# Kernel optimization log

Hardware: AMD Instinct MI355X
Metric: run time of the kernel (lower is better)

## Reference

```python
import jax, jax.numpy as jnp
import numpy as np

SIGMAS = [15, 80, 250]  # hardcoded defaults in retinex_MSR


def _gauss_k1d(sigma):
    # matches get_gauss_kernel(sigma, dim=1)
    ksize = int(np.floor(sigma * 6) / 2) * 2 + 1
    k = np.arange(ksize, dtype=np.float32) - ksize // 2
    k = np.exp(-k ** 2 / (2.0 * sigma ** 2))
    k /= k.sum()
    return jnp.asarray(k)


def _gauss_blur(x, k1d):
    # x: (N, 1, H, W); separable blur with zero padding, same as F.conv2d
    K = k1d.shape[0]
    pad = K // 2
    dn = ('NCHW', 'OIHW', 'NCHW')
    kv = k1d.reshape(1, 1, K, 1)
    kh = k1d.reshape(1, 1, 1, K)
    x = jax.lax.conv_general_dilated(x, kv, (1, 1), [(pad, pad), (0, 0)], dimension_numbers=dn)
    x = jax.lax.conv_general_dilated(x, kh, (1, 1), [(0, 0), (pad, pad)], dimension_numbers=dn)
    return x


def setup_inputs() -> dict:
    key = jax.random.key(0)
    img = jax.random.uniform(key, (16, 3, 512, 512), dtype=jnp.float32)
    return {"img": img}


def reference(img):
    B, C, H, W = img.shape
    # all channels processed identically as single-channel depthwise convs:
    # fold channels into batch for one big conv per sigma
    x = img.astype(jnp.float32).reshape(B * C, 1, H, W)
    w = 1.0 / len(SIGMAS)  # default equal weights summing to 1
    r = jnp.zeros((B * C, 1, H, W), dtype=jnp.float32)
    for sigma in SIGMAS:
        r = r + jnp.log(_gauss_blur(x, _gauss_k1d(sigma)) + 1.0) * w
    r = r.reshape(B, C, H, W)
    # per-channel min-max stretch, global over batch and spatial dims
    mmin = r.min(axis=(0, 2, 3), keepdims=True)
    mmax = r.max(axis=(0, 2, 3), keepdims=True)
    return (r - mmin) / (mmax - mmin)
```

## Files before the change

### kernel.cpp

```cpp
#include <hip/hip_runtime.h>
#include <math.h>


#define NSL 48

#define W0_OFF 0
#define W1_OFF 512
#define W2_OFF 1280
#define MM_OFF 2816
#define G16_BYTE_OFF 16384
#define X16_BYTE_OFF 1589248
#define T16_BYTE_OFF 26755072

typedef _Float16 half8 __attribute__((ext_vector_type(8)));
typedef float f32x4 __attribute__((ext_vector_type(4)));

__device__ __forceinline__ void gload16(const void* g, void* l) {
  __builtin_amdgcn_global_load_lds(
      (const __attribute__((address_space(1))) void*)g,
      (__attribute__((address_space(3))) void*)l, 16, 0, 0);
}

#define WAITV4() asm volatile("s_waitcnt vmcnt(4)" ::: "memory")
#define WAITV0() asm volatile("s_waitcnt vmcnt(0)" ::: "memory")
#define SCHEDB() __builtin_amdgcn_sched_barrier(0)
#define BARRIER() __builtin_amdgcn_s_barrier()

__global__ void wkern(float* __restrict__ ws) {
  __shared__ float red[256];
  const int s = blockIdx.x;
  const int Ks[3] = {91, 481, 1501};
  const float sg[3] = {15.f, 80.f, 250.f};
  const int off[3] = {W0_OFF, W1_OFF, W2_OFF};
  const int alloc[3] = {512, 768, 1536};
  const int K = Ks[s], A = alloc[s];
  float* wb = ws + off[s];
  const int t = threadIdx.x;
  for (int i = t; i < A; i += 256) wb[i] = 0.f;
  __syncthreads();
  const float inv2s2 = 1.f / (2.f * sg[s] * sg[s]);
  float part = 0.f;
  for (int i = t; i < K; i += 256) {
    const float d = (float)(i - K / 2);
    const float e = __expf(-d * d * inv2s2);
    wb[16 + i] = e;
    part += e;
  }
  red[t] = part;
  __syncthreads();
  for (int st = 128; st > 0; st >>= 1) {
    if (t < st) red[t] += red[t + st];
    __syncthreads();
  }
  const float inv = 1.f / red[0];
  for (int i = t; i < K; i += 256) wb[16 + i] *= inv;
}

__global__ void mm_init(unsigned* __restrict__ mm) {
  const int t = threadIdx.x;
  if (t < 3) mm[t] = 0xFFFFFFFFu;
  else if (t < 6) mm[t] = 0u;
}

__global__ void gkern(const float* __restrict__ ws, _Float16* __restrict__ gb) {
  const int y = blockIdx.x;
  const int s = blockIdx.y;
  const int Rs[3] = {45, 240, 750};
  const int off[3] = {W0_OFF, W1_OFF, W2_OFF};
  const float* w = ws + off[s] + 16;
  _Float16* g = gb + ((size_t)s << 18) + ((size_t)y << 9);
  const int R = Rs[s], K = 2 * R + 1;
  for (int x = threadIdx.x; x < 512; x += 256) {
    const int i = x - y + R;
    const float v = (i >= 0 && i < K) ? w[i] : 0.f;
    g[x] = (_Float16)v;
  }
}

__global__ __launch_bounds__(256) void xconv(const float* __restrict__ X,
                                             _Float16* __restrict__ X16) {
  const size_t i = ((size_t)blockIdx.x * 256 + threadIdx.x) << 3;
  const float4 v0 = *reinterpret_cast<const float4*>(X + i);
  const float4 v1 = *reinterpret_cast<const float4*>(X + i + 4);
  half8 h;
  h[0] = (_Float16)v0.x; h[1] = (_Float16)v0.y;
  h[2] = (_Float16)v0.z; h[3] = (_Float16)v0.w;
  h[4] = (_Float16)v1.x; h[5] = (_Float16)v1.y;
  h[6] = (_Float16)v1.z; h[7] = (_Float16)v1.w;
  *reinterpret_cast<half8*>(X16 + i) = h;
}

#define STAGE_P(buf)                                 \
  do {                                               \
    gload16(pA0, &As[buf][t << 3]);                  \
    gload16(pA1, &As[buf][(256 + t) << 3]);          \
    gload16(pB0, &Bs[buf][t << 3]);                  \
    gload16(pB1, &Bs[buf][(256 + t) << 3]);          \
    pA0 += 32; pA1 += 32; pB0 += 32; pB1 += 32;      \
  } while (0)

#define FRAGS_AND_MFMA(buf)                                                         \
  do {                                                                              \
    half8 af[4], bf[4];                                                             \
    _Pragma("unroll") for (int f = 0; f < 4; ++f) {                                 \
      af[f] = *reinterpret_cast<const half8*>(                                      \
          &As[buf][(((wr << 6) + (f << 4) + lr) << 5) + (lg << 3)]);                \
      bf[f] = *reinterpret_cast<const half8*>(                                      \
          &Bs[buf][(((wc << 6) + (f << 4) + lr) << 5) + (lg << 3)]);                \
    }                                                                               \
    _Pragma("unroll") for (int fm = 0; fm < 4; ++fm)                                \
        _Pragma("unroll") for (int fn = 0; fn < 4; ++fn)                            \
        acc[fm][fn] = __builtin_amdgcn_mfma_f32_16x16x32_f16(af[fm], bf[fn],        \
                                                             acc[fm][fn], 0, 0, 0); \
  } while (0)

#define K_PIPELINE_LOOP()                                                           \
  do {                                                                              \
    const int row_ = t >> 2;                                                        \
    const int c8_ = (t & 3) << 3;                                                   \
    const _Float16* pA0 =                                                           \
        Ap + ((size_t)(bm + row_) << 9) + (klo << 5) + c8_;                         \
    const _Float16* pA1 = pA0 + ((size_t)64 << 9);                                  \
    const _Float16* pB0 =                                                           \
        Bp + ((size_t)(bn + row_) << 9) + (klo << 5) + c8_;                         \
    const _Float16* pB1 = pB0 + ((size_t)64 << 9);                                  \
    STAGE_P(0);                                                                     \
    STAGE_P(1);                                                                     \
    int cb = 0;                                                                     \
    for (int kt = klo; kt <= khi; ++kt) {                                           \
      if (kt < khi) { WAITV4(); } else { WAITV0(); }                                \
      SCHEDB();                                                                     \
      BARRIER();                                                                    \
      SCHEDB();                                                                     \
      if (kt + 2 <= khi) {                                                          \
        const int sb = (cb + 2 >= 3) ? cb - 1 : cb + 2;                             \
        STAGE_P(sb);                                                                \
      }                                                                             \
      FRAGS_AND_MFMA(cb);                                                           \
      cb = (cb == 2) ? 0 : cb + 1;                                                  \
    }                                                                               \
  } while (0)

__global__ __launch_bounds__(256) void gemm1_k(const _Float16* __restrict__ X16,
                                               const _Float16* __restrict__ G16,
                                               _Float16* __restrict__ T16) {
  __shared__ __align__(16) _Float16 As[3][128 * 32];
  __shared__ __align__(16) _Float16 Bs[3][128 * 32];
  const int t = threadIdx.x;
  const int lane = t & 63, wave = t >> 6;
  const int wr = wave >> 1, wc = wave & 1;
  const int lr = lane & 15, lg = lane >> 4;
  const int idx = blockIdx.x;
  const int idy = blockIdx.y;
  const int idx12 = idy % 12;
  const int q = idx + ((idy / 12) << 3);
  const int bn = (q & 3) << 7;
  const int slice = q >> 2;
  const int bm = (idx12 & 3) << 7;
  const int s = idx12 >> 2;
  const int Rs[3] = {45, 240, 750};
  const int R = Rs[s];
  const _Float16* Ap = G16 + ((size_t)s << 18);
  const _Float16* Bp = X16 + ((size_t)slice << 18);
  _Float16* Tout = T16 + ((size_t)(s * NSL + slice) << 18);

  int klo = bm - R;
  klo = (klo > 0 ? klo : 0) >> 5;
  int khi = bm + 127 + R;
  if (khi > 511) khi = 511;
  khi >>= 5;

  f32x4 acc[4][4];
#pragma unroll
  for (int i = 0; i < 4; ++i)
#pragma unroll
    for (int j = 0; j < 4; ++j) acc[i][j] = (f32x4){0.f, 0.f, 0.f, 0.f};

  K_PIPELINE_LOOP();

#pragma unroll
  for (int fm = 0; fm < 4; ++fm)
#pragma unroll
    for (int fn = 0; fn < 4; ++fn) {
      const int a0 = bm + (wr << 6) + (fm << 4) + (lg << 2);
      const int b0 = bn + (wc << 6) + (fn << 4) + lr;
#pragma unroll
      for (int j = 0; j < 4; ++j)
        Tout[((size_t)(a0 + j) << 9) + b0] = (_Float16)acc[fm][fn][j];
    }
}

__global__ __launch_bounds__(256) void gemm2_k(const _Float16* __restrict__ G16,
                                               const _Float16* __restrict__ T16,
                                               float* __restrict__ out,
                                               unsigned* __restrict__ mm) {
  __shared__ __align__(16) _Float16 As[3][128 * 32];
  __shared__ __align__(16) _Float16 Bs[3][128 * 32];
  __shared__ float smn[4], smx[4];
  const int t = threadIdx.x;
  const int lane = t & 63, wave = t >> 6;
  const int wr = wave >> 1, wc = wave & 1;
  const int lr = lane & 15, lg = lane >> 4;
  const int idx = blockIdx.x;
  const int idy = blockIdx.y;
  const int bm = (idy & 3) << 7;
  const int q = idx + ((idy >> 2) << 3);
  const int bn = (q & 3) << 7;
  const int slice = q >> 2;
  const float w3 = 1.f / 3.f;
  const int Rs[3] = {45, 240, 750};

  f32x4 res[4][4];
#pragma unroll
  for (int i = 0; i < 4; ++i)
#pragma unroll
    for (int j = 0; j < 4; ++j) res[i][j] = (f32x4){0.f, 0.f, 0.f, 0.f};

#pragma unroll 1
  for (int s = 0; s < 3; ++s) {
    const int R = Rs[s];
    const _Float16* Ap = G16 + ((size_t)s << 18);
    const _Float16* Bp = T16 + ((size_t)(s * NSL + slice) << 18);
    int klo = bm - R;
    klo = (klo > 0 ? klo : 0) >> 5;
    int khi = bm + 127 + R;
    if (khi > 511) khi = 511;
    khi >>= 5;

    f32x4 acc[4][4];
#pragma unroll
    for (int i = 0; i < 4; ++i)
#pragma unroll
      for (int j = 0; j < 4; ++j) acc[i][j] = (f32x4){0.f, 0.f, 0.f, 0.f};

    BARRIER();
    K_PIPELINE_LOOP();

#pragma unroll
    for (int fm = 0; fm < 4; ++fm)
#pragma unroll
      for (int fn = 0; fn < 4; ++fn)
#pragma unroll
        for (int j = 0; j < 4; ++j)
          res[fm][fn][j] += w3 * __logf(acc[fm][fn][j] + 1.f);
  }

  float mn = 3.4e38f, mx = -3.4e38f;
#pragma unroll
  for (int fm = 0; fm < 4; ++fm)
#pragma unroll
    for (int fn = 0; fn < 4; ++fn) {
      const int rb = bm + (wr << 6) + (fm << 4) + (lg << 2);
      const int cg = bn + (wc << 6) + (fn << 4) + lr;
      float* op = out + ((size_t)slice << 18) + ((size_t)rb << 9) + cg;
#pragma unroll
      for (int j = 0; j < 4; ++j) {
        const float v = res[fm][fn][j];
        op[j << 9] = v;
        mn = fminf(mn, v);
        mx = fmaxf(mx, v);
      }
    }
#pragma unroll
  for (int off = 32; off > 0; off >>= 1) {
    mn = fminf(mn, __shfl_xor(mn, off));
    mx = fmaxf(mx, __shfl_xor(mx, off));
  }
  if (lane == 0) {
    smn[wave] = mn;
    smx[wave] = mx;
  }
  __syncthreads();
  if (t == 0) {
    mn = fminf(fminf(smn[0], smn[1]), fminf(smn[2], smn[3]));
    mx = fmaxf(fmaxf(smx[0], smx[1]), fmaxf(smx[2], smx[3]));
    const int ch = slice % 3;
    atomicMin(&mm[ch], __float_as_uint(mn));
    atomicMax(&mm[3 + ch], __float_as_uint(mx));
  }
}

__global__ __launch_bounds__(256) void norm_k(float* __restrict__ r,
                                              const unsigned* __restrict__ mm) {
  const int b = blockIdx.x;
  const int slice = b >> 4;
  const int piece = b & 15;
  const int ch = slice % 3;
  const float mn = __uint_as_float(mm[ch]);
  const float mx = __uint_as_float(mm[3 + ch]);
  const float inv = 1.f / (mx - mn);
  float* p = r + ((size_t)slice << 18) + (piece << 14);
  const int t = threadIdx.x;
  for (int q = 0; q < 16; ++q) {
    float4 v = *reinterpret_cast<const float4*>(&p[(q * 256 + t) << 2]);
    v.x = (v.x - mn) * inv;
    v.y = (v.y - mn) * inv;
    v.z = (v.z - mn) * inv;
    v.w = (v.w - mn) * inv;
    *reinterpret_cast<float4*>(&p[(q * 256 + t) << 2]) = v;
  }
}

extern "C" void kernel_launch(void* const* d_in, const int* in_sizes, int n_in,
                              void* d_out, int out_size, void* d_ws, size_t ws_size,
                              hipStream_t stream) {
  const float* img = (const float*)d_in[0];
  float* out = (float*)d_out;
  float* wsf = (float*)d_ws;
  unsigned* mm = (unsigned*)(wsf + MM_OFF);
  _Float16* G16 = (_Float16*)((char*)d_ws + G16_BYTE_OFF);
  _Float16* X16 = (_Float16*)((char*)d_ws + X16_BYTE_OFF);
  _Float16* T16 = (_Float16*)((char*)d_ws + T16_BYTE_OFF);

  wkern<<<3, 256, 0, stream>>>(wsf);
  mm_init<<<1, 64, 0, stream>>>(mm);
  gkern<<<dim3(512, 3), 256, 0, stream>>>(wsf, G16);
  xconv<<<6144, 256, 0, stream>>>(img, X16);

  gemm1_k<<<dim3(8, 288), 256, 0, stream>>>(X16, G16, T16);
  gemm2_k<<<dim3(8, 96), 256, 0, stream>>>(G16, T16, out, mm);

  norm_k<<<768, 256, 0, stream>>>(out, mm);
}
```

Before: 156.6 us.

## Switch GEMM K-loop to 64-wide tiles with double buffering and syncthreads

The banded GEMM K-loop now stages 64-wide K tiles instead of 32-wide ones, using two LDS buffers in place of three. The manual vmcnt waits and sched barriers are replaced by a plain __syncthreads each iteration. This halves the number of loop iterations and barriers per tile, which cuts per-iteration overhead. In exchange it loses the deeper prefetch, shares one barrier between the wait and the next load, and makes the band edges coarser, so some extra zero-weight K work is done.

```diff
diff --git a/kernel.cpp b/kernel.cpp
--- a/kernel.cpp
+++ b/kernel.cpp
@@ -20,11 +20,6 @@
       (const __attribute__((address_space(1))) void*)g,
       (__attribute__((address_space(3))) void*)l, 16, 0, 0);
 }
-
-#define WAITV4() asm volatile("s_waitcnt vmcnt(4)" ::: "memory")
-#define WAITV0() asm volatile("s_waitcnt vmcnt(0)" ::: "memory")
-#define SCHEDB() __builtin_amdgcn_sched_barrier(0)
-#define BARRIER() __builtin_amdgcn_s_barrier()
 
 __global__ void wkern(float* __restrict__ ws) {
   __shared__ float red[256];
@@ -90,62 +85,64 @@
   *reinterpret_cast<half8*>(X16 + i) = h;
 }
 
-#define STAGE_P(buf)                                 \
-  do {                                               \
-    gload16(pA0, &As[buf][t << 3]);                  \
-    gload16(pA1, &As[buf][(256 + t) << 3]);          \
-    gload16(pB0, &Bs[buf][t << 3]);                  \
-    gload16(pB1, &Bs[buf][(256 + t) << 3]);          \
-    pA0 += 32; pA1 += 32; pB0 += 32; pB1 += 32;      \
+#define STAGE8(buf)                                    \
+  do {                                                 \
+    gload16(pA0, &As[buf][t << 3]);                    \
+    gload16(pA1, &As[buf][(256 + t) << 3]);            \
+    gload16(pA2, &As[buf][(512 + t) << 3]);            \
+    gload16(pA3, &As[buf][(768 + t) << 3]);            \
+    gload16(pB0, &Bs[buf][t << 3]);                    \
+    gload16(pB1, &Bs[buf][(256 + t) << 3]);            \
+    gload16(pB2, &Bs[buf][(512 + t) << 3]);            \
+    gload16(pB3, &Bs[buf][(768 + t) << 3]);            \
+    pA0 += 64; pA1 += 64; pA2 += 64; pA3 += 64;        \
+    pB0 += 64; pB1 += 64; pB2 += 64; pB3 += 64;        \
   } while (0)
 
 #define FRAGS_AND_MFMA(buf)                                                         \
   do {                                                                              \
-    half8 af[4], bf[4];                                                             \
-    _Pragma("unroll") for (int f = 0; f < 4; ++f) {                                 \
-      af[f] = *reinterpret_cast<const half8*>(                                      \
-          &As[buf][(((wr << 6) + (f << 4) + lr) << 5) + (lg << 3)]);                \
-      bf[f] = *reinterpret_cast<const half8*>(                                      \
-          &Bs[buf][(((wc << 6) + (f << 4) + lr) << 5) + (lg << 3)]);                \
+    _Pragma("unroll") for (int ks = 0; ks < 2; ++ks) {                              \
+      half8 af[4], bf[4];                                                           \
+      _Pragma("unroll") for (int f = 0; f < 4; ++f) {                               \
+        af[f] = *reinterpret_cast<const half8*>(                                    \
+            &As[buf][(((wr << 6) + (f << 4) + lr) << 6) + (ks << 5) + (lg << 3)]);  \
+        bf[f] = *reinterpret_cast<const half8*>(                                    \
+            &Bs[buf][(((wc << 6) + (f << 4) + lr) << 6) + (ks << 5) + (lg << 3)]);  \
+      }                                                                             \
+      _Pragma("unroll") for (int fm = 0; fm < 4; ++fm)                              \
+          _Pragma("unroll") for (int fn = 0; fn < 4; ++fn)                          \
+          acc[fm][fn] = __builtin_amdgcn_mfma_f32_16x16x32_f16(af[fm], bf[fn],      \
+                                                               acc[fm][fn], 0, 0, 0); \
     }                                                                               \
-    _Pragma("unroll") for (int fm = 0; fm < 4; ++fm)                                \
-        _Pragma("unroll") for (int fn = 0; fn < 4; ++fn)                            \
-        acc[fm][fn] = __builtin_amdgcn_mfma_f32_16x16x32_f16(af[fm], bf[fn],        \
-                                                             acc[fm][fn], 0, 0, 0); \
   } while (0)
 
 #define K_PIPELINE_LOOP()                                                           \
   do {                                                                              \
-    const int row_ = t >> 2;                                                        \
-    const int c8_ = (t & 3) << 3;                                                   \
-    const _Float16* pA0 =                                                           \
-        Ap + ((size_t)(bm + row_) << 9) + (klo << 5) + c8_;                         \
-    const _Float16* pA1 = pA0 + ((size_t)64 << 9);                                  \
-    const _Float16* pB0 =                                                           \
-        Bp + ((size_t)(bn + row_) << 9) + (klo << 5) + c8_;                         \
-    const _Float16* pB1 = pB0 + ((size_t)64 << 9);                                  \
-    STAGE_P(0);                                                                     \
-    STAGE_P(1);                                                                     \
+    const int rA_ = t >> 3;                                                         \
+    const int g8_ = (t & 7) << 3;                                                   \
+    const _Float16* pA0 = Ap + ((size_t)(bm + rA_) << 9) + (klo << 6) + g8_;        \
+    const _Float16* pA1 = pA0 + ((size_t)32 << 9);                                  \
+    const _Float16* pA2 = pA0 + ((size_t)64 << 9);                                  \
+    const _Float16* pA3 = pA0 + ((size_t)96 << 9);                                  \
+    const _Float16* pB0 = Bp + ((size_t)(bn + rA_) << 9) + (klo << 6) + g8_;        \
+    const _Float16* pB1 = pB0 + ((size_t)32 << 9);                                  \
+    const _Float16* pB2 = pB0 + ((size_t)64 << 9);                                  \
+    const _Float16* pB3 = pB0 + ((size_t)96 << 9);                                  \
+    STAGE8(0);                                                                      \
     int cb = 0;                                                                     \
     for (int kt = klo; kt <= khi; ++kt) {                                           \
-      if (kt < khi) { WAITV4(); } else { WAITV0(); }                                \
-      SCHEDB();                                                                     \
-      BARRIER();                                                                    \
-      SCHEDB();                                                                     \
-      if (kt + 2 <= khi) {                                                          \
-        const int sb = (cb + 2 >= 3) ? cb - 1 : cb + 2;                             \
-        STAGE_P(sb);                                                                \
-      }                                                                             \
+      __syncthreads();                                                              \
+      if (kt < khi) STAGE8(cb ^ 1);                                                 \
       FRAGS_AND_MFMA(cb);                                                           \
-      cb = (cb == 2) ? 0 : cb + 1;                                                  \
+      cb ^= 1;                                                                      \
     }                                                                               \
   } while (0)
 
 __global__ __launch_bounds__(256) void gemm1_k(const _Float16* __restrict__ X16,
                                                const _Float16* __restrict__ G16,
                                                _Float16* __restrict__ T16) {
-  __shared__ __align__(16) _Float16 As[3][128 * 32];
-  __shared__ __align__(16) _Float16 Bs[3][128 * 32];
+  __shared__ __align__(16) _Float16 As[2][128 * 64];
+  __shared__ __align__(16) _Float16 Bs[2][128 * 64];
   const int t = threadIdx.x;
   const int lane = t & 63, wave = t >> 6;
   const int wr = wave >> 1, wc = wave & 1;
@@ -165,10 +162,10 @@
   _Float16* Tout = T16 + ((size_t)(s * NSL + slice) << 18);
 
   int klo = bm - R;
-  klo = (klo > 0 ? klo : 0) >> 5;
+  klo = (klo > 0 ? klo : 0) >> 6;
   int khi = bm + 127 + R;
   if (khi > 511) khi = 511;
-  khi >>= 5;
+  khi >>= 6;
 
   f32x4 acc[4][4];
 #pragma unroll
@@ -194,8 +191,8 @@
                                                const _Float16* __restrict__ T16,
                                                float* __restrict__ out,
                                                unsigned* __restrict__ mm) {
-  __shared__ __align__(16) _Float16 As[3][128 * 32];
-  __shared__ __align__(16) _Float16 Bs[3][128 * 32];
+  __shared__ __align__(16) _Float16 As[2][128 * 64];
+  __shared__ __align__(16) _Float16 Bs[2][128 * 64];
   __shared__ float smn[4], smx[4];
   const int t = threadIdx.x;
   const int lane = t & 63, wave = t >> 6;
@@ -222,10 +219,10 @@
     const _Float16* Ap = G16 + ((size_t)s << 18);
     const _Float16* Bp = T16 + ((size_t)(s * NSL + slice) << 18);
     int klo = bm - R;
-    klo = (klo > 0 ? klo : 0) >> 5;
+    klo = (klo > 0 ? klo : 0) >> 6;
     int khi = bm + 127 + R;
     if (khi > 511) khi = 511;
-    khi >>= 5;
+    khi >>= 6;
 
     f32x4 acc[4][4];
 #pragma unroll
@@ -233,7 +230,7 @@
 #pragma unroll
       for (int j = 0; j < 4; ++j) acc[i][j] = (f32x4){0.f, 0.f, 0.f, 0.f};
 
-    BARRIER();
+    __syncthreads();
     K_PIPELINE_LOOP();
 
 #pragma unroll
```

Result: slower. 165.4 us (+5.6%).

## Use 64-wide K tiles with XOR-swizzled LDS and double buffering in gemm2

Applied to the files above, without the earlier changes.

The second banded GEMM now stages K tiles of 64 instead of 32, double-buffered instead of triple-buffered. Global-to-LDS loads use an XOR-swizzled column chunk so fragment reads avoid LDS bank conflicts. Explicit vmcnt waits are replaced by plain __syncthreads. This halves the barrier count per K range and cuts bank conflicts, but the band bounds are coarser (more zero-band work), LDS use rises to 64KB, and only one tile of prefetch is in flight.

```diff
diff --git a/kernel.cpp b/kernel.cpp
--- a/kernel.cpp
+++ b/kernel.cpp
@@ -90,7 +90,7 @@
   *reinterpret_cast<half8*>(X16 + i) = h;
 }
 
-#define STAGE_P(buf)                                 \
+#define STAGE_P1(buf)                                \
   do {                                               \
     gload16(pA0, &As[buf][t << 3]);                  \
     gload16(pA1, &As[buf][(256 + t) << 3]);          \
@@ -99,7 +99,7 @@
     pA0 += 32; pA1 += 32; pB0 += 32; pB1 += 32;      \
   } while (0)
 
-#define FRAGS_AND_MFMA(buf)                                                         \
+#define FRAGS_MFMA1(buf)                                                            \
   do {                                                                              \
     half8 af[4], bf[4];                                                             \
     _Pragma("unroll") for (int f = 0; f < 4; ++f) {                                 \
@@ -114,7 +114,7 @@
                                                              acc[fm][fn], 0, 0, 0); \
   } while (0)
 
-#define K_PIPELINE_LOOP()                                                           \
+#define K_LOOP1()                                                                   \
   do {                                                                              \
     const int row_ = t >> 2;                                                        \
     const int c8_ = (t & 3) << 3;                                                   \
@@ -124,8 +124,8 @@
     const _Float16* pB0 =                                                           \
         Bp + ((size_t)(bn + row_) << 9) + (klo << 5) + c8_;                         \
     const _Float16* pB1 = pB0 + ((size_t)64 << 9);                                  \
-    STAGE_P(0);                                                                     \
-    STAGE_P(1);                                                                     \
+    STAGE_P1(0);                                                                    \
+    STAGE_P1(1);                                                                    \
     int cb = 0;                                                                     \
     for (int kt = klo; kt <= khi; ++kt) {                                           \
       if (kt < khi) { WAITV4(); } else { WAITV0(); }                                \
@@ -134,9 +134,9 @@
       SCHEDB();                                                                     \
       if (kt + 2 <= khi) {                                                          \
         const int sb = (cb + 2 >= 3) ? cb - 1 : cb + 2;                             \
-        STAGE_P(sb);                                                                \
+        STAGE_P1(sb);                                                               \
       }                                                                             \
-      FRAGS_AND_MFMA(cb);                                                           \
+      FRAGS_MFMA1(cb);                                                              \
       cb = (cb == 2) ? 0 : cb + 1;                                                  \
     }                                                                               \
   } while (0)
@@ -176,7 +176,7 @@
 #pragma unroll
     for (int j = 0; j < 4; ++j) acc[i][j] = (f32x4){0.f, 0.f, 0.f, 0.f};
 
-  K_PIPELINE_LOOP();
+  K_LOOP1();
 
 #pragma unroll
   for (int fm = 0; fm < 4; ++fm)
@@ -189,13 +189,68 @@
         Tout[((size_t)(a0 + j) << 9) + b0] = (_Float16)acc[fm][fn][j];
     }
 }
+
+#define STAGE8SW(buf)                                  \
+  do {                                                 \
+    gload16(pA0, &As[buf][t << 3]);                    \
+    gload16(pA1, &As[buf][(256 + t) << 3]);            \
+    gload16(pA2, &As[buf][(512 + t) << 3]);            \
+    gload16(pA3, &As[buf][(768 + t) << 3]);            \
+    gload16(pB0, &Bs[buf][t << 3]);                    \
+    gload16(pB1, &Bs[buf][(256 + t) << 3]);            \
+    gload16(pB2, &Bs[buf][(512 + t) << 3]);            \
+    gload16(pB3, &Bs[buf][(768 + t) << 3]);            \
+    pA0 += 64; pA1 += 64; pA2 += 64; pA3 += 64;        \
+    pB0 += 64; pB1 += 64; pB2 += 64; pB3 += 64;        \
+  } while (0)
+
+#define FRAGS_MFMA2(buf)                                                            \
+  do {                                                                              \
+    _Pragma("unroll") for (int ks = 0; ks < 2; ++ks) {                              \
+      half8 af[4], bf[4];                                                           \
+      _Pragma("unroll") for (int f = 0; f < 4; ++f) {                               \
+        af[f] = *reinterpret_cast<const half8*>(                                    \
+            &As[buf][(((wr << 6) + (f << 4) + lr) << 6) +                           \
+                     ((((ks << 2) + lg) ^ (lr & 7)) << 3)]);                        \
+        bf[f] = *reinterpret_cast<const half8*>(                                    \
+            &Bs[buf][(((wc << 6) + (f << 4) + lr) << 6) +                           \
+                     ((((ks << 2) + lg) ^ (lr & 7)) << 3)]);                        \
+      }                                                                             \
+      _Pragma("unroll") for (int fm = 0; fm < 4; ++fm)                              \
+          _Pragma("unroll") for (int fn = 0; fn < 4; ++fn)                          \
+          acc[fm][fn] = __builtin_amdgcn_mfma_f32_16x16x32_f16(af[fm], bf[fn],      \
+                                                               acc[fm][fn], 0, 0, 0); \
+    }                                                                               \
+  } while (0)
+
+#define K_LOOP2()                                                                   \
+  do {                                                                              \
+    const int rA_ = t >> 3;                                                         \
+    const int gsw_ = ((t & 7) ^ ((t >> 3) & 7)) << 3;      \
+    const _Float16* pA0 = Ap + ((size_t)(bm + rA_) << 9) + (klo << 6) + gsw_;       \
+    const _Float16* pA1 = pA0 + ((size_t)32 << 9);                                  \
+    const _Float16* pA2 = pA0 + ((size_t)64 << 9);                                  \
+    const _Float16* pA3 = pA0 + ((size_t)96 << 9);                                  \
+    const _Float16* pB0 = Bp + ((size_t)(bn + rA_) << 9) + (klo << 6) + gsw_;       \
+    const _Float16* pB1 = pB0 + ((size_t)32 << 9);                                  \
+    const _Float16* pB2 = pB0 + ((size_t)64 << 9);                                  \
+    const _Float16* pB3 = pB0 + ((size_t)96 << 9);                                  \
+    STAGE8SW(0);                                                                    \
+    int cb = 0;                                                                     \
+    for (int kt = klo; kt <= khi; ++kt) {                                           \
+      __syncthreads();                                                              \
+      if (kt < khi) STAGE8SW(cb ^ 1);                                               \
+      FRAGS_MFMA2(cb);                                                              \
+      cb ^= 1;                                                                      \
+    }                                                                               \
+  } while (0)
 
 __global__ __launch_bounds__(256) void gemm2_k(const _Float16* __restrict__ G16,
                                                const _Float16* __restrict__ T16,
                                                float* __restrict__ out,
                                                unsigned* __restrict__ mm) {
-  __shared__ __align__(16) _Float16 As[3][128 * 32];
-  __shared__ __align__(16) _Float16 Bs[3][128 * 32];
+  __shared__ __align__(16) _Float16 As[2][128 * 64];
+  __shared__ __align__(16) _Float16 Bs[2][128 * 64];
   __shared__ float smn[4], smx[4];
   const int t = threadIdx.x;
   const int lane = t & 63, wave = t >> 6;
@@ -222,10 +277,10 @@
     const _Float16* Ap = G16 + ((size_t)s << 18);
     const _Float16* Bp = T16 + ((size_t)(s * NSL + slice) << 18);
     int klo = bm - R;
-    klo = (klo > 0 ? klo : 0) >> 5;
+    klo = (klo > 0 ? klo : 0) >> 6;
     int khi = bm + 127 + R;
     if (khi > 511) khi = 511;
-    khi >>= 5;
+    khi >>= 6;
 
     f32x4 acc[4][4];
 #pragma unroll
@@ -233,8 +288,8 @@
 #pragma unroll
       for (int j = 0; j < 4; ++j) acc[i][j] = (f32x4){0.f, 0.f, 0.f, 0.f};
 
-    BARRIER();
-    K_PIPELINE_LOOP();
+    __syncthreads();
+    K_LOOP2();
 
 #pragma unroll
     for (int fm = 0; fm < 4; ++fm)
```

After: 147.6 us. -5.7%, faster.
